# Performance work log

Measured on AMD Instinct MI355X. Metric: run time of the kernel, lower is better.

The kernel has to match this reference:

```python
import jax, jax.numpy as jnp
import numpy as np

BETA = 1.0
B, S, D = 4, 4096, 1024


def setup_inputs() -> dict:
    key = jax.random.key(0)
    k_x, k_q, k_k, k_v = jax.random.split(key, 4)
    scale = 1.0 / np.sqrt(D)  # nn.Linear-like init scale
    x = jax.random.normal(k_x, (B, S, D), dtype=jnp.float32)
    Wq = jax.random.uniform(k_q, (D, D), dtype=jnp.float32, minval=-scale, maxval=scale)
    Wk = jax.random.uniform(k_k, (D, D), dtype=jnp.float32, minval=-scale, maxval=scale)
    Wv = jax.random.uniform(k_v, (D, D), dtype=jnp.float32, minval=-scale, maxval=scale)
    return {"x": x, "Wq": Wq, "Wk": Wk, "Wv": Wv}


def reference(x, Wq, Wk, Wv):
    # nn.Linear(bias=False): y = x @ W.T
    q = jnp.einsum('bsd,ed->bse', x, Wq)
    k = jnp.einsum('bsd,ed->bse', x, Wk)
    v = jnp.einsum('bsd,ed->bse', x, Wv)
    scores = jnp.einsum('bqd,bkd->bqk', q, k)          # [B, S, S]
    attn = jax.nn.softmax(BETA * scores, axis=-1)
    attended = jnp.einsum('bqk,bkd->bqd', attn, v)
    y = attended + x
    return y / jnp.linalg.norm(y, axis=-1, keepdims=True)
```

## Files before the change

kernel.cpp:

```cpp
#include <hip/hip_runtime.h>
#include <hip/hip_bf16.h>

typedef unsigned short u16;
typedef unsigned int   u32;
typedef _Float16 half8 __attribute__((ext_vector_type(8)));
typedef __attribute__((ext_vector_type(4))) float f32x4;

constexpr int NB = 4;
constexpr int S  = 4096;
constexpr int D  = 1024;
constexpr int BK = 64;

__device__ __forceinline__ u16 h2u(_Float16 h) {
    union { _Float16 h; u16 u; } v; v.h = h; return v.u;
}

__device__ __forceinline__ void async16(const void* g, void* l) {
    __builtin_amdgcn_global_load_lds(
        (const __attribute__((address_space(1))) unsigned int*)g,
        (__attribute__((address_space(3))) unsigned int*)l, 16, 0, 0);
}

__device__ __forceinline__ void gemm_nt_async(
    const u16* __restrict__ A, const u16* __restrict__ B, int K,
    u16* As, u16* Bs, f32x4 acc[4][4])
{
    const int tid  = threadIdx.x;
    const int lane = tid & 63;
    const int wid  = tid >> 6;
    const int quad = lane >> 4;
    const int lrow = lane & 15;
    const int s7   = lrow & 7;
    const int wm   = (wid & 1) * 64;
    const int wn   = (wid >> 1) * 64;

    const int rl = lane >> 3;
    const int cl = lane & 7;
    const int gc = cl ^ rl;
    const int row0 = wid * 32 + rl;
    const u16* Ag = A + (size_t)row0 * K + gc * 8;
    const u16* Bg = B + (size_t)row0 * K + gc * 8;
    u16* Al = As + ((size_t)wid * 256 + lane) * 8;
    u16* Bl = Bs + ((size_t)wid * 256 + lane) * 8;

    for (int k0 = 0; k0 < K; k0 += BK) {
        __syncthreads();
#pragma unroll
        for (int j = 0; j < 4; ++j)
            async16(Ag + k0 + (size_t)j * 8 * K, Al + j * 512);
#pragma unroll
        for (int j = 0; j < 4; ++j)
            async16(Bg + k0 + (size_t)j * 8 * K, Bl + j * 512);
        __syncthreads();
#pragma unroll
        for (int kk = 0; kk < 2; ++kk) {
            half8 af[4], bf[4];
#pragma unroll
            for (int i = 0; i < 4; ++i)
                af[i] = *(const half8*)(As + (wm + i * 16 + lrow) * 64
                                           + (((kk * 4 + quad) ^ s7) * 8));
#pragma unroll
            for (int i = 0; i < 4; ++i)
                bf[i] = *(const half8*)(Bs + (wn + i * 16 + lrow) * 64
                                           + (((kk * 4 + quad) ^ s7) * 8));
#pragma unroll
            for (int im = 0; im < 4; ++im)
#pragma unroll
                for (int in = 0; in < 4; ++in)
                    acc[im][in] = __builtin_amdgcn_mfma_f32_16x16x32_f16(
                        af[im], bf[in], acc[im][in], 0, 0, 0);
        }
    }
}

__global__ __launch_bounds__(256) void cvt_kernel(
    const float* __restrict__ in, u16* __restrict__ out, int n8)
{
    const int i = blockIdx.x * 256 + threadIdx.x;
    if (i >= n8) return;
    const float4 a = *(const float4*)(in + (size_t)i * 8);
    const float4 b = *(const float4*)(in + (size_t)i * 8 + 4);
    half8 h;
    h[0] = (_Float16)a.x; h[1] = (_Float16)a.y;
    h[2] = (_Float16)a.z; h[3] = (_Float16)a.w;
    h[4] = (_Float16)b.x; h[5] = (_Float16)b.y;
    h[6] = (_Float16)b.z; h[7] = (_Float16)b.w;
    *(half8*)(out + (size_t)i * 8) = h;
}

__global__ __launch_bounds__(256) void qkv_kernel(
    const u16* __restrict__ x16, const u16* __restrict__ W16,
    u16* __restrict__ Q, u16* __restrict__ Kb, u16* __restrict__ V)
{
    __shared__ __align__(16) u16 As[128 * BK];
    __shared__ __align__(16) u16 Bs[128 * BK];
    const int tile_m = blockIdx.x * 128;
    const int tile_n = blockIdx.y * 128;
    const u16* W = W16 + (size_t)blockIdx.z * D * D;
    u16* out = (blockIdx.z == 0) ? Q : (blockIdx.z == 1) ? Kb : V;

    f32x4 acc[4][4];
#pragma unroll
    for (int i = 0; i < 4; ++i)
#pragma unroll
        for (int j = 0; j < 4; ++j) acc[i][j] = (f32x4)0.0f;

    gemm_nt_async(x16 + (size_t)tile_m * D, W + (size_t)tile_n * D, D, As, Bs, acc);

    const int tid = threadIdx.x, lane = tid & 63, wid = tid >> 6;
    const int quad = lane >> 4, lrow = lane & 15;
    const int wm = (wid & 1) * 64, wn = (wid >> 1) * 64;
#pragma unroll
    for (int im = 0; im < 4; ++im)
#pragma unroll
        for (int r = 0; r < 4; ++r) {
            const int row = tile_m + wm + im * 16 + quad * 4 + r;
#pragma unroll
            for (int in = 0; in < 4; ++in) {
                const int col = tile_n + wn + in * 16 + lrow;
                out[(size_t)row * D + col] = h2u((_Float16)acc[im][in][r]);
            }
        }
}

__global__ __launch_bounds__(256) void transpose_v(
    const u16* __restrict__ V, u16* __restrict__ Vt)
{
    __shared__ u16 t[64][72];
    const int sg = blockIdx.x * 64;
    const int b  = sg >> 12;
    const int s0 = sg & (S - 1);
    const int e0 = blockIdx.y * 64;
    const int tid = threadIdx.x;
#pragma unroll
    for (int p = 0; p < 2; ++p) {
        const int v  = tid + 256 * p;
        const int sr = v >> 3, sc = (v & 7) * 8;
        half8 vec = *(const half8*)(V + (size_t)(sg + sr) * D + e0 + sc);
        *(half8*)&t[sr][sc] = vec;
    }
    __syncthreads();
#pragma unroll
    for (int p = 0; p < 2; ++p) {
        const int v  = tid + 256 * p;
        const int e  = v >> 3, s8 = (v & 7) * 8;
        u16 o[8];
#pragma unroll
        for (int j = 0; j < 8; ++j) o[j] = t[s8 + j][e];
        *(uint4*)(Vt + (size_t)b * D * S + (size_t)(e0 + e) * S + s0 + s8) = *(const uint4*)o;
    }
}

__global__ __launch_bounds__(256) void scores_kernel(
    const u16* __restrict__ Q, const u16* __restrict__ Kb, u16* __restrict__ P)
{
    __shared__ __align__(16) u16 As[128 * BK];
    __shared__ __align__(16) u16 Bs[128 * BK];
    const int b = blockIdx.z;
    const int tile_m = blockIdx.x * 128;
    const int tile_n = blockIdx.y * 128;
    const u16* Ab = Q  + (size_t)b * S * D + (size_t)tile_m * D;
    const u16* Bv = Kb + (size_t)b * S * D + (size_t)tile_n * D;

    f32x4 acc[4][4];
#pragma unroll
    for (int i = 0; i < 4; ++i)
#pragma unroll
        for (int j = 0; j < 4; ++j) acc[i][j] = (f32x4)0.0f;

    gemm_nt_async(Ab, Bv, D, As, Bs, acc);

    u16* Pb = P + (size_t)b * S * S;
    const int tid = threadIdx.x, lane = tid & 63, wid = tid >> 6;
    const int quad = lane >> 4, lrow = lane & 15;
    const int wm = (wid & 1) * 64, wn = (wid >> 1) * 64;
#pragma unroll
    for (int im = 0; im < 4; ++im)
#pragma unroll
        for (int r = 0; r < 4; ++r) {
            const int row = tile_m + wm + im * 16 + quad * 4 + r;
#pragma unroll
            for (int in = 0; in < 4; ++in) {
                const int col = tile_n + wn + in * 16 + lrow;
                Pb[(size_t)row * S + col] = h2u((_Float16)acc[im][in][r]);
            }
        }
}

__global__ __launch_bounds__(256) void softmax_kernel(u16* __restrict__ P)
{
    const size_t row = blockIdx.x;
    u16* p = P + row * S;
    const int tid = threadIdx.x;

    half8 h0 = *(const half8*)(p + tid * 16);
    half8 h1 = *(const half8*)(p + tid * 16 + 8);
    float v[16];
#pragma unroll
    for (int i = 0; i < 8; ++i) { v[i] = (float)h0[i]; v[8 + i] = (float)h1[i]; }

    float m = v[0];
#pragma unroll
    for (int i = 1; i < 16; ++i) m = fmaxf(m, v[i]);
#pragma unroll
    for (int off = 32; off > 0; off >>= 1) m = fmaxf(m, __shfl_xor(m, off));

    __shared__ float redm[4], reds[4];
    const int wid = tid >> 6;
    if ((tid & 63) == 0) redm[wid] = m;
    __syncthreads();
    m = fmaxf(fmaxf(redm[0], redm[1]), fmaxf(redm[2], redm[3]));

    float e[16], s = 0.f;
#pragma unroll
    for (int i = 0; i < 16; ++i) { e[i] = __expf(v[i] - m); s += e[i]; }
#pragma unroll
    for (int off = 32; off > 0; off >>= 1) s += __shfl_xor(s, off);
    if ((tid & 63) == 0) reds[wid] = s;
    __syncthreads();
    s = reds[0] + reds[1] + reds[2] + reds[3];
    const float inv = 1.0f / s;

#pragma unroll
    for (int i = 0; i < 8; ++i) {
        h0[i] = (_Float16)(e[i] * inv);
        h1[i] = (_Float16)(e[8 + i] * inv);
    }
    *(half8*)(p + tid * 16)     = h0;
    *(half8*)(p + tid * 16 + 8) = h1;
}

__global__ __launch_bounds__(256) void pv_kernel(
    const u16* __restrict__ P, const u16* __restrict__ Vt,
    const float* __restrict__ x, float* __restrict__ y)
{
    __shared__ __align__(16) u16 As[128 * BK];
    __shared__ __align__(16) u16 Bs[128 * BK];
    const int b = blockIdx.z;
    const int tile_m = blockIdx.x * 128;
    const int tile_n = blockIdx.y * 128;
    const u16* Ab = P  + (size_t)b * S * S + (size_t)tile_m * S;
    const u16* Bv = Vt + (size_t)b * D * S + (size_t)tile_n * S;

    f32x4 acc[4][4];
#pragma unroll
    for (int i = 0; i < 4; ++i)
#pragma unroll
        for (int j = 0; j < 4; ++j) acc[i][j] = (f32x4)0.0f;

    gemm_nt_async(Ab, Bv, S, As, Bs, acc);

    const int tid = threadIdx.x, lane = tid & 63, wid = tid >> 6;
    const int quad = lane >> 4, lrow = lane & 15;
    const int wm = (wid & 1) * 64, wn = (wid >> 1) * 64;

#pragma unroll
    for (int im = 0; im < 4; ++im)
#pragma unroll
        for (int r = 0; r < 4; ++r) {
            const int row = tile_m + wm + im * 16 + quad * 4 + r;
            const size_t base = ((size_t)b * S + row) * D;
#pragma unroll
            for (int in = 0; in < 4; ++in) {
                const int col = tile_n + wn + in * 16 + lrow;
                y[base + col] = acc[im][in][r] + x[base + col];
            }
        }
}

__global__ __launch_bounds__(256) void normalize_kernel(float* __restrict__ y)
{
    const size_t row = blockIdx.x;
    const int tid = threadIdx.x;
    float4* p = (float4*)(y + row * D) + tid;

    float4 v = *p;
    float ss = v.x * v.x + v.y * v.y + v.z * v.z + v.w * v.w;
#pragma unroll
    for (int off = 32; off > 0; off >>= 1) ss += __shfl_xor(ss, off);

    __shared__ float red[4];
    const int wid = tid >> 6;
    if ((tid & 63) == 0) red[wid] = ss;
    __syncthreads();
    const float inv = rsqrtf(red[0] + red[1] + red[2] + red[3]);

    v.x *= inv; v.y *= inv; v.z *= inv; v.w *= inv;
    *p = v;
}

extern "C" void kernel_launch(void* const* d_in, const int* in_sizes, int n_in,
                              void* d_out, int out_size, void* d_ws, size_t ws_size,
                              hipStream_t stream) {
    const float* x  = (const float*)d_in[0];
    const float* Wq = (const float*)d_in[1];
    const float* Wk = (const float*)d_in[2];
    const float* Wv = (const float*)d_in[3];
    float* out = (float*)d_out;

    char* ws = (char*)d_ws;
    const size_t MB = 1ull << 20;
    u16* Q   = (u16*)(ws);
    u16* Kb  = (u16*)(ws + 32 * MB);
    u16* Vt  = (u16*)(ws + 64 * MB);
    u16* P   = (u16*)(ws + 96 * MB);
    u16* V   = P;
    u16* x16 = Vt;
    u16* W16 = (u16*)(ws + 218 * MB);

    dim3 blk(256);
    cvt_kernel <<<dim3(NB * S * D / 8 / 256), blk, 0, stream>>>(x,  x16, NB * S * D / 8);
    cvt_kernel <<<dim3(D * D / 8 / 256), blk, 0, stream>>>(Wq, W16,             D * D / 8);
    cvt_kernel <<<dim3(D * D / 8 / 256), blk, 0, stream>>>(Wk, W16 + (size_t)D * D, D * D / 8);
    cvt_kernel <<<dim3(D * D / 8 / 256), blk, 0, stream>>>(Wv, W16 + (size_t)2 * D * D, D * D / 8);

    qkv_kernel    <<<dim3(NB * S / 128, D / 128, 3), blk, 0, stream>>>(x16, W16, Q, Kb, V);
    transpose_v   <<<dim3(NB * S / 64, D / 64), blk, 0, stream>>>(V, Vt);
    scores_kernel <<<dim3(S / 128, S / 128, NB), blk, 0, stream>>>(Q, Kb, P);
    softmax_kernel<<<dim3(NB * S), blk, 0, stream>>>(P);
    pv_kernel     <<<dim3(S / 128, D / 128, NB), blk, 0, stream>>>(P, Vt, x, out);
    normalize_kernel<<<dim3(NB * S), blk, 0, stream>>>(out);
}
```

Before: 614.0 us.

## Replace GEMM core with 256x256 tiles, double-buffered async LDS pipeline

The shared GEMM routine moves from 128x128 tiles with single-buffered LDS and two full barriers per K step to 256x256 tiles computed by 512-thread blocks (8 waves). Global-to-LDS async loads are double-buffered and issued in quarter pieces interleaved with MFMA phases, using explicit vmcnt waits, barriers, sched_barrier fences and s_setprio. The aim is to hide global load latency behind MFMA work and raise arithmetic intensity per block for the QKV, scores and PV matmuls. In exchange it uses 128KB of LDS per block, more accumulator registers, and coarser grids that leave fewer blocks for the QKV and PV launches.

```diff
diff --git a/kernel.cpp b/kernel.cpp
--- a/kernel.cpp
+++ b/kernel.cpp
@@ -1,15 +1,12 @@
 #include <hip/hip_runtime.h>
-#include <hip/hip_bf16.h>
 
 typedef unsigned short u16;
-typedef unsigned int   u32;
 typedef _Float16 half8 __attribute__((ext_vector_type(8)));
 typedef __attribute__((ext_vector_type(4))) float f32x4;
 
 constexpr int NB = 4;
 constexpr int S  = 4096;
 constexpr int D  = 1024;
-constexpr int BK = 64;
 
 __device__ __forceinline__ u16 h2u(_Float16 h) {
     union { _Float16 h; u16 u; } v; v.h = h; return v.u;
@@ -21,55 +18,111 @@
         (__attribute__((address_space(3))) unsigned int*)l, 16, 0, 0);
 }
 
-__device__ __forceinline__ void gemm_nt_async(
-    const u16* __restrict__ A, const u16* __restrict__ B, int K,
-    u16* As, u16* Bs, f32x4 acc[4][4])
+#define BAR()  __builtin_amdgcn_s_barrier()
+#define SFEN() __builtin_amdgcn_sched_barrier(0)
+
+#define MF(AF, BF, QM, QN)                                                     \
+  do {                                                                         \
+    _Pragma("unroll") for (int m_ = 0; m_ < 4; ++m_)                           \
+    _Pragma("unroll") for (int n_ = 0; n_ < 2; ++n_)                           \
+    _Pragma("unroll") for (int k_ = 0; k_ < 2; ++k_)                           \
+      acc[(QM)*4 + m_][(QN)*2 + n_] = __builtin_amdgcn_mfma_f32_16x16x32_f16(  \
+          AF[m_][k_], BF[n_][k_], acc[(QM)*4 + m_][(QN)*2 + n_], 0, 0, 0);     \
+  } while (0)
+
+#define GHALF(RA, RB, OA, OB, KO, KN)                                          \
+  {                                               \
+    _Pragma("unroll") for (int m_ = 0; m_ < 4; ++m_) {                         \
+      a0[m_][0] = rdA(RA, 0, m_, 0); a0[m_][1] = rdA(RA, 0, m_, 1); }          \
+    _Pragma("unroll") for (int n_ = 0; n_ < 2; ++n_) {                         \
+      b0[n_][0] = rdB(RB, 0, n_, 0); b0[n_][1] = rdB(RB, 0, n_, 1); }          \
+    issue(Am, OA, rsA + 64, KO);                                               \
+    BAR();                                                                     \
+    __builtin_amdgcn_s_setprio(1); MF(a0, b0, 0, 0);                           \
+    __builtin_amdgcn_s_setprio(0);                                             \
+    asm volatile("s_waitcnt vmcnt(6)" ::: "memory");                           \
+    BAR(); SFEN();                                                             \
+                                                  \
+    _Pragma("unroll") for (int n_ = 0; n_ < 2; ++n_) {                         \
+      b1[n_][0] = rdB(RB, 1, n_, 0); b1[n_][1] = rdB(RB, 1, n_, 1); }          \
+    issue(Bm, OB, rsB + 32, KO);                                               \
+    BAR();                                                                     \
+    __builtin_amdgcn_s_setprio(1); MF(a0, b1, 0, 1);                           \
+    __builtin_amdgcn_s_setprio(0);                                             \
+    BAR(); SFEN();                                                             \
+                                                  \
+    _Pragma("unroll") for (int m_ = 0; m_ < 4; ++m_) {                         \
+      a1[m_][0] = rdA(RA, 1, m_, 0); a1[m_][1] = rdA(RA, 1, m_, 1); }          \
+    issue(Am, RA, rsA, KN);                                                    \
+    BAR();                                                                     \
+    __builtin_amdgcn_s_setprio(1); MF(a1, b0, 1, 0);                           \
+    __builtin_amdgcn_s_setprio(0);                                             \
+    BAR(); SFEN();                                                             \
+                                                  \
+    issue(Bm, RB, rsB, KN);                                                    \
+    BAR();                                                                     \
+    __builtin_amdgcn_s_setprio(1); MF(a1, b1, 1, 1);                           \
+    __builtin_amdgcn_s_setprio(0);                                             \
+    asm volatile("s_waitcnt vmcnt(8)" ::: "memory");                           \
+    BAR(); SFEN();                                                             \
+  }
+
+__device__ __forceinline__ void gemm256(
+    const u16* __restrict__ Am, const u16* __restrict__ Bm, const int K,
+    u16* lds, f32x4 acc[8][4])
 {
     const int tid  = threadIdx.x;
     const int lane = tid & 63;
-    const int wid  = tid >> 6;
+    const int w    = tid >> 6;
+    const int wm   = w >> 2;
+    const int wn   = w & 3;
     const int quad = lane >> 4;
     const int lrow = lane & 15;
     const int s7   = lrow & 7;
-    const int wm   = (wid & 1) * 64;
-    const int wn   = (wid >> 1) * 64;
-
-    const int rl = lane >> 3;
-    const int cl = lane & 7;
-    const int gc = cl ^ rl;
-    const int row0 = wid * 32 + rl;
-    const u16* Ag = A + (size_t)row0 * K + gc * 8;
-    const u16* Bg = B + (size_t)row0 * K + gc * 8;
-    u16* Al = As + ((size_t)wid * 256 + lane) * 8;
-    u16* Bl = Bs + ((size_t)wid * 256 + lane) * 8;
-
-    for (int k0 = 0; k0 < K; k0 += BK) {
-        __syncthreads();
-#pragma unroll
-        for (int j = 0; j < 4; ++j)
-            async16(Ag + k0 + (size_t)j * 8 * K, Al + j * 512);
-#pragma unroll
-        for (int j = 0; j < 4; ++j)
-            async16(Bg + k0 + (size_t)j * 8 * K, Bl + j * 512);
-        __syncthreads();
-#pragma unroll
-        for (int kk = 0; kk < 2; ++kk) {
-            half8 af[4], bf[4];
-#pragma unroll
-            for (int i = 0; i < 4; ++i)
-                af[i] = *(const half8*)(As + (wm + i * 16 + lrow) * 64
-                                           + (((kk * 4 + quad) ^ s7) * 8));
-#pragma unroll
-            for (int i = 0; i < 4; ++i)
-                bf[i] = *(const half8*)(Bs + (wn + i * 16 + lrow) * 64
-                                           + (((kk * 4 + quad) ^ s7) * 8));
-#pragma unroll
-            for (int im = 0; im < 4; ++im)
-#pragma unroll
-                for (int in = 0; in < 4; ++in)
-                    acc[im][in] = __builtin_amdgcn_mfma_f32_16x16x32_f16(
-                        af[im], bf[in], acc[im][in], 0, 0, 0);
-        }
+    const int rl   = lane >> 3;
+    const int gc8  = ((lane & 7) ^ rl) * 8;
+    const int rsA  = ((w >> 2) << 7) + ((w & 3) << 4);
+    const int rsB  = ((w >> 1) << 6) + ((w & 1) << 4);
+
+    u16* const As0 = lds;
+    u16* const Bs0 = lds + 16384;
+    u16* const As1 = lds + 32768;
+    u16* const Bs1 = lds + 49152;
+
+    auto issue = [&](const u16* M, u16* dst, int rs, int k0) {
+        async16(M + (size_t)(rs + rl) * K + k0 + gc8,
+                dst + (size_t)(rs)     * 64 + (size_t)lane * 8);
+        async16(M + (size_t)(rs + 8 + rl) * K + k0 + gc8,
+                dst + (size_t)(rs + 8) * 64 + (size_t)lane * 8);
+    };
+    auto rdA = [&](const u16* buf, int qm, int m, int kk) -> half8 {
+        return *(const half8*)(buf + (wm * 128 + qm * 64 + m * 16 + lrow) * 64
+                                   + (((kk << 2) + quad) ^ s7) * 8);
+    };
+    auto rdB = [&](const u16* buf, int qn, int n, int kk) -> half8 {
+        return *(const half8*)(buf + (wn * 64 + qn * 32 + n * 16 + lrow) * 64
+                                   + (((kk << 2) + quad) ^ s7) * 8);
+    };
+
+    issue(Am, As0, rsA,      0);
+    issue(Bm, Bs0, rsB,      0);
+    issue(Am, As0, rsA + 64, 0);
+    issue(Bm, Bs0, rsB + 32, 0);
+    issue(Am, As1, rsA,      64);
+    issue(Bm, Bs1, rsB,      64);
+    asm volatile("s_waitcnt vmcnt(8)" ::: "memory");
+    BAR(); SFEN();
+
+    half8 a0[4][2], a1[4][2], b0[2][2], b1[2][2];
+    const int kmask = K - 1;
+    const int NI = K >> 7;
+    for (int it = 0; it < NI; ++it) {
+        const int kb  = it << 7;
+        const int t1k = (kb + 64)  & kmask;
+        const int t2k = (kb + 128) & kmask;
+        const int t3k = (kb + 192) & kmask;
+        GHALF(As0, Bs0, As1, Bs1, t1k, t2k)
+        GHALF(As1, Bs1, As0, Bs0, t2k, t3k)
     }
 }
 
@@ -88,37 +141,36 @@
     *(half8*)(out + (size_t)i * 8) = h;
 }
 
-__global__ __launch_bounds__(256) void qkv_kernel(
+__global__ __launch_bounds__(512, 2) void qkv_kernel(
     const u16* __restrict__ x16, const u16* __restrict__ W16,
     u16* __restrict__ Q, u16* __restrict__ Kb, u16* __restrict__ V)
 {
-    __shared__ __align__(16) u16 As[128 * BK];
-    __shared__ __align__(16) u16 Bs[128 * BK];
-    const int tile_m = blockIdx.x * 128;
-    const int tile_n = blockIdx.y * 128;
+    __shared__ __align__(16) u16 lds[65536];
+    const int tile_m = blockIdx.x * 256;
+    const int tile_n = blockIdx.y * 256;
     const u16* W = W16 + (size_t)blockIdx.z * D * D;
     u16* out = (blockIdx.z == 0) ? Q : (blockIdx.z == 1) ? Kb : V;
 
-    f32x4 acc[4][4];
-#pragma unroll
-    for (int i = 0; i < 4; ++i)
+    f32x4 acc[8][4];
+#pragma unroll
+    for (int i = 0; i < 8; ++i)
 #pragma unroll
         for (int j = 0; j < 4; ++j) acc[i][j] = (f32x4)0.0f;
 
-    gemm_nt_async(x16 + (size_t)tile_m * D, W + (size_t)tile_n * D, D, As, Bs, acc);
-
-    const int tid = threadIdx.x, lane = tid & 63, wid = tid >> 6;
+    gemm256(x16 + (size_t)tile_m * D, W + (size_t)tile_n * D, D, lds, acc);
+
+    const int tid = threadIdx.x, lane = tid & 63, w = tid >> 6;
     const int quad = lane >> 4, lrow = lane & 15;
-    const int wm = (wid & 1) * 64, wn = (wid >> 1) * 64;
-#pragma unroll
-    for (int im = 0; im < 4; ++im)
+    const int wm = w >> 2, wn = w & 3;
+#pragma unroll
+    for (int mi = 0; mi < 8; ++mi)
 #pragma unroll
         for (int r = 0; r < 4; ++r) {
-            const int row = tile_m + wm + im * 16 + quad * 4 + r;
-#pragma unroll
-            for (int in = 0; in < 4; ++in) {
-                const int col = tile_n + wn + in * 16 + lrow;
-                out[(size_t)row * D + col] = h2u((_Float16)acc[im][in][r]);
+            const int row = tile_m + wm * 128 + mi * 16 + quad * 4 + r;
+#pragma unroll
+            for (int ni = 0; ni < 4; ++ni) {
+                const int col = tile_n + wn * 64 + ni * 16 + lrow;
+                out[(size_t)row * D + col] = h2u((_Float16)acc[mi][ni][r]);
             }
         }
 }
@@ -151,38 +203,37 @@
     }
 }
 
-__global__ __launch_bounds__(256) void scores_kernel(
+__global__ __launch_bounds__(512, 2) void scores_kernel(
     const u16* __restrict__ Q, const u16* __restrict__ Kb, u16* __restrict__ P)
 {
-    __shared__ __align__(16) u16 As[128 * BK];
-    __shared__ __align__(16) u16 Bs[128 * BK];
+    __shared__ __align__(16) u16 lds[65536];
     const int b = blockIdx.z;
-    const int tile_m = blockIdx.x * 128;
-    const int tile_n = blockIdx.y * 128;
+    const int tile_m = blockIdx.x * 256;
+    const int tile_n = blockIdx.y * 256;
     const u16* Ab = Q  + (size_t)b * S * D + (size_t)tile_m * D;
     const u16* Bv = Kb + (size_t)b * S * D + (size_t)tile_n * D;
 
-    f32x4 acc[4][4];
-#pragma unroll
-    for (int i = 0; i < 4; ++i)
+    f32x4 acc[8][4];
+#pragma unroll
+    for (int i = 0; i < 8; ++i)
 #pragma unroll
         for (int j = 0; j < 4; ++j) acc[i][j] = (f32x4)0.0f;
 
-    gemm_nt_async(Ab, Bv, D, As, Bs, acc);
+    gemm256(Ab, Bv, D, lds, acc);
 
     u16* Pb = P + (size_t)b * S * S;
-    const int tid = threadIdx.x, lane = tid & 63, wid = tid >> 6;
+    const int tid = threadIdx.x, lane = tid & 63, w = tid >> 6;
     const int quad = lane >> 4, lrow = lane & 15;
-    const int wm = (wid & 1) * 64, wn = (wid >> 1) * 64;
-#pragma unroll
-    for (int im = 0; im < 4; ++im)
+    const int wm = w >> 2, wn = w & 3;
+#pragma unroll
+    for (int mi = 0; mi < 8; ++mi)
 #pragma unroll
         for (int r = 0; r < 4; ++r) {
-            const int row = tile_m + wm + im * 16 + quad * 4 + r;
-#pragma unroll
-            for (int in = 0; in < 4; ++in) {
-                const int col = tile_n + wn + in * 16 + lrow;
-                Pb[(size_t)row * S + col] = h2u((_Float16)acc[im][in][r]);
+            const int row = tile_m + wm * 128 + mi * 16 + quad * 4 + r;
+#pragma unroll
+            for (int ni = 0; ni < 4; ++ni) {
+                const int col = tile_n + wn * 64 + ni * 16 + lrow;
+                Pb[(size_t)row * S + col] = h2u((_Float16)acc[mi][ni][r]);
             }
         }
 }
@@ -230,40 +281,39 @@
     *(half8*)(p + tid * 16 + 8) = h1;
 }
 
-__global__ __launch_bounds__(256) void pv_kernel(
+__global__ __launch_bounds__(512, 2) void pv_kernel(
     const u16* __restrict__ P, const u16* __restrict__ Vt,
     const float* __restrict__ x, float* __restrict__ y)
 {
-    __shared__ __align__(16) u16 As[128 * BK];
-    __shared__ __align__(16) u16 Bs[128 * BK];
+    __shared__ __align__(16) u16 lds[65536];
     const int b = blockIdx.z;
-    const int tile_m = blockIdx.x * 128;
-    const int tile_n = blockIdx.y * 128;
+    const int tile_m = blockIdx.x * 256;
+    const int tile_n = blockIdx.y * 256;
     const u16* Ab = P  + (size_t)b * S * S + (size_t)tile_m * S;
     const u16* Bv = Vt + (size_t)b * D * S + (size_t)tile_n * S;
 
-    f32x4 acc[4][4];
-#pragma unroll
-    for (int i = 0; i < 4; ++i)
+    f32x4 acc[8][4];
+#pragma unroll
+    for (int i = 0; i < 8; ++i)
 #pragma unroll
         for (int j = 0; j < 4; ++j) acc[i][j] = (f32x4)0.0f;
 
-    gemm_nt_async(Ab, Bv, S, As, Bs, acc);
-
-    const int tid = threadIdx.x, lane = tid & 63, wid = tid >> 6;
+    gemm256(Ab, Bv, S, lds, acc);
+
+    const int tid = threadIdx.x, lane = tid & 63, w = tid >> 6;
     const int quad = lane >> 4, lrow = lane & 15;
-    const int wm = (wid & 1) * 64, wn = (wid >> 1) * 64;
-
-#pragma unroll
-    for (int im = 0; im < 4; ++im)
+    const int wm = w >> 2, wn = w & 3;
+
+#pragma unroll
+    for (int mi = 0; mi < 8; ++mi)
 #pragma unroll
         for (int r = 0; r < 4; ++r) {
-            const int row = tile_m + wm + im * 16 + quad * 4 + r;
+            const int row = tile_m + wm * 128 + mi * 16 + quad * 4 + r;
             const size_t base = ((size_t)b * S + row) * D;
 #pragma unroll
-            for (int in = 0; in < 4; ++in) {
-                const int col = tile_n + wn + in * 16 + lrow;
-                y[base + col] = acc[im][in][r] + x[base + col];
+            for (int ni = 0; ni < 4; ++ni) {
+                const int col = tile_n + wn * 64 + ni * 16 + lrow;
+                y[base + col] = acc[mi][ni][r] + x[base + col];
             }
         }
 }
@@ -309,15 +359,16 @@
     u16* W16 = (u16*)(ws + 218 * MB);
 
     dim3 blk(256);
+    dim3 blk2(512);
     cvt_kernel <<<dim3(NB * S * D / 8 / 256), blk, 0, stream>>>(x,  x16, NB * S * D / 8);
     cvt_kernel <<<dim3(D * D / 8 / 256), blk, 0, stream>>>(Wq, W16,             D * D / 8);
     cvt_kernel <<<dim3(D * D / 8 / 256), blk, 0, stream>>>(Wk, W16 + (size_t)D * D, D * D / 8);
     cvt_kernel <<<dim3(D * D / 8 / 256), blk, 0, stream>>>(Wv, W16 + (size_t)2 * D * D, D * D / 8);
 
-    qkv_kernel    <<<dim3(NB * S / 128, D / 128, 3), blk, 0, stream>>>(x16, W16, Q, Kb, V);
+    qkv_kernel    <<<dim3(NB * S / 256, D / 256, 3), blk2, 0, stream>>>(x16, W16, Q, Kb, V);
     transpose_v   <<<dim3(NB * S / 64, D / 64), blk, 0, stream>>>(V, Vt);
-    scores_kernel <<<dim3(S / 128, S / 128, NB), blk, 0, stream>>>(Q, Kb, P);
+    scores_kernel <<<dim3(S / 256, S / 256, NB), blk2, 0, stream>>>(Q, Kb, P);
     softmax_kernel<<<dim3(NB * S), blk, 0, stream>>>(P);
-    pv_kernel     <<<dim3(S / 128, D / 128, NB), blk, 0, stream>>>(P, Vt, x, out);
+    pv_kernel     <<<dim3(S / 256, D / 256, NB), blk2, 0, stream>>>(P, Vt, x, out);
     normalize_kernel<<<dim3(NB * S), blk, 0, stream>>>(out);
 }
```

New measurement: 537.8 us. -12.4%, faster.
